# Kernel tuning notes

Hardware: AMD Instinct MI355X
Metric: run time of the kernel (lower is better)

The kernel has to match this reference:

```python
import jax, jax.numpy as jnp
import numpy as np

N_NODES = 100000
N_EDGES = 1600000  # undirected edges (each pair listed once, no self loops)
IN_CH, HID, OUT_CH = 512, 64, 32
MU, P, K = 0.1, 1.5, 2
EPS = 1e-8


def setup_inputs() -> dict:
    key = jax.random.key(0)
    k_x, k_src, k_off, k_w1, k_w2 = jax.random.split(key, 5)
    x = jax.random.normal(k_x, (N_NODES, IN_CH), dtype=jnp.float32)
    # undirected edge list with no self loops: dst = (src + offset) % N, offset in [1, N)
    src = jax.random.randint(k_src, (N_EDGES,), 0, N_NODES)
    off = jax.random.randint(k_off, (N_EDGES,), 1, N_NODES)
    dst = (src + off) % N_NODES
    edge_index = jnp.stack([src, dst], axis=0)
    # parameters (lin1 of pGNNNet, lin1 of pGNNConv)
    W1 = jax.random.normal(k_w1, (IN_CH, HID), dtype=jnp.float32) / np.sqrt(IN_CH)
    b1 = jnp.zeros((HID,), dtype=jnp.float32)
    W2 = jax.random.normal(k_w2, (HID, OUT_CH), dtype=jnp.float32) / np.sqrt(HID)
    b2 = jnp.zeros((OUT_CH,), dtype=jnp.float32)
    return {"x": x, "edge_index": edge_index, "W1": W1, "b1": b1, "W2": W2, "b2": b2}


def reference(x, edge_index, W1, b1, W2, b2):
    src, dst = edge_index[0], edge_index[1]
    n = x.shape[0]
    # pGNNNet.lin1 + ReLU (dropout is identity in eval mode)
    h = jax.nn.relu(x @ W1 + b1)                   # [N, HID]
    # pGNNConv.lin1 applied before propagation
    f = h @ W2 + b2                                # [N, OUT]
    # degrees of the symmetric adjacency (no self loops)
    ones = jnp.ones(src.shape, dtype=f.dtype)
    deg = jax.ops.segment_sum(ones, src, num_segments=n) + \
          jax.ops.segment_sum(ones, dst, num_segments=n)
    dinv = jnp.where(deg > 0, 1.0 / deg, 0.0)      # [N]
    dis = jnp.sqrt(dinv)                           # D^{-1/2}
    out = f
    for _ in range(K):
        gs = out * dis[:, None]                    # D^{-1/2} f
        g = gs[src] - gs[dst]                      # graph gradient per edge [E, OUT]
        # edge reweighting: ||grad||^{p-2}
        w = jnp.power(jnp.sum(g * g, axis=1) + EPS, (P - 2.0) * 0.5)   # [E]
        # row sums of M (symmetric, M_ij = w_e)
        s = jax.ops.segment_sum(w, src, num_segments=n) + \
            jax.ops.segment_sum(w, dst, num_segments=n)
        alpha = 1.0 / (s * dinv + MU)              # [N]
        beta = MU * alpha
        # (D^{-1/2} M D^{-1/2} out): scatter-add messages both directions
        m = w[:, None]
        agg = jax.ops.segment_sum(m * gs[dst], src, num_segments=n) + \
              jax.ops.segment_sum(m * gs[src], dst, num_segments=n)
        out = alpha[:, None] * (dis[:, None] * agg) + beta[:, None] * f
    return jax.nn.log_softmax(out, axis=1)
```

## Files before the change

kernel.cpp:

```cpp
#include <hip/hip_runtime.h>
#include <hip/hip_bf16.h>
#include <math.h>

#define N_NODES 100000
#define N_EDGES 1600000
#define IN_CH 512
#define HID 64
#define OUT_CH 32
#define MU 0.1f
#define EPS 1e-8f

#define HE (2 * N_EDGES)
#define ABLK 625
#define EPT 20
#define NBUCK 391

typedef short bf16x8 __attribute__((ext_vector_type(8)));
typedef unsigned short us8 __attribute__((ext_vector_type(8)));
typedef float f32x4 __attribute__((ext_vector_type(4)));

__device__ __forceinline__ short f2bf(float f) {
  __hip_bfloat16 h = __float2bfloat16(f);
  return *reinterpret_cast<short*>(&h);
}
__device__ __forceinline__ float bf2f(unsigned short u) {
  unsigned int b = ((unsigned int)u) << 16;
  return __uint_as_float(b);
}

__global__ void k_prep(const float* __restrict__ W1, const float* __restrict__ W2,
                       short* __restrict__ w1t, short* __restrict__ w2t) {
  int i = blockIdx.x * 256 + threadIdx.x;
  if (i < IN_CH * HID) {
    int k = i / HID, c = i % HID;
    w1t[c * IN_CH + k] = f2bf(W1[i]);
  } else if (i < IN_CH * HID + HID * OUT_CH) {
    int j = i - IN_CH * HID;
    int k = j / OUT_CH, c = j % OUT_CH;
    w2t[c * HID + k] = f2bf(W2[j]);
  }
}

__global__ __launch_bounds__(256) void k_mlp(
    const float* __restrict__ x, const short* __restrict__ w1t,
    const float* __restrict__ b1, const short* __restrict__ w2t,
    const float* __restrict__ b2, const int* __restrict__ deg,
    float* __restrict__ f, unsigned short* __restrict__ gs) {
  __shared__ short ht[4][16][72];

  const int t = threadIdx.x;
  const int w = t >> 6;
  const int l = t & 63;
  const int lr = l & 15;
  const int kq = l >> 4;

  const int band = blockIdx.x * 64 + w * 16;
  const int gr = band + lr;
  const int grl = gr < N_NODES ? gr : N_NODES - 1;

  f32x4 acc1[4] = {};
  const float* xrow = x + (size_t)grl * IN_CH + kq * 8;
  #pragma unroll 4
  for (int ksub = 0; ksub < 16; ++ksub) {
    float4 alo = *(const float4*)(xrow + ksub * 32);
    float4 ahi = *(const float4*)(xrow + ksub * 32 + 4);
    bf16x8 a;
    a[0] = f2bf(alo.x); a[1] = f2bf(alo.y); a[2] = f2bf(alo.z); a[3] = f2bf(alo.w);
    a[4] = f2bf(ahi.x); a[5] = f2bf(ahi.y); a[6] = f2bf(ahi.z); a[7] = f2bf(ahi.w);
    #pragma unroll
    for (int ct = 0; ct < 4; ++ct) {
      const int c = ct * 16 + lr;
      bf16x8 b = *(const bf16x8*)&w1t[c * IN_CH + ksub * 32 + kq * 8];
      acc1[ct] = __builtin_amdgcn_mfma_f32_16x16x32_bf16(a, b, acc1[ct], 0, 0, 0);
    }
  }

  #pragma unroll
  for (int ct = 0; ct < 4; ++ct) {
    const int c = ct * 16 + lr;
    const float bb = b1[c];
    #pragma unroll
    for (int r = 0; r < 4; ++r) {
      float h = acc1[ct][r] + bb;
      ht[w][kq * 4 + r][c] = f2bf(h > 0.f ? h : 0.f);
    }
  }
  __syncthreads();

  f32x4 acc2[2] = {};
  #pragma unroll
  for (int ks = 0; ks < 2; ++ks) {
    bf16x8 a2 = *(const bf16x8*)&ht[w][lr][ks * 32 + kq * 8];
    #pragma unroll
    for (int ct = 0; ct < 2; ++ct) {
      const int c = ct * 16 + lr;
      bf16x8 b = *(const bf16x8*)&w2t[c * HID + ks * 32 + kq * 8];
      acc2[ct] = __builtin_amdgcn_mfma_f32_16x16x32_bf16(a2, b, acc2[ct], 0, 0, 0);
    }
  }

  #pragma unroll
  for (int r = 0; r < 4; ++r) {
    const int gr2 = band + kq * 4 + r;
    if (gr2 < N_NODES) {
      const int d = deg[gr2];
      const float di = d > 0 ? 1.0f / (float)d : 0.0f;
      const float disv = sqrtf(di);
      #pragma unroll
      for (int ct = 0; ct < 2; ++ct) {
        const int c = ct * 16 + lr;
        const float fv = acc2[ct][r] + b2[c];
        f[(size_t)gr2 * OUT_CH + c] = fv;
        gs[(size_t)gr2 * OUT_CH + c] = (unsigned short)f2bf(fv * disv);
      }
    }
  }
}

__global__ __launch_bounds__(256) void k_bcount(const int* __restrict__ ends,
                                                int* __restrict__ bcnt) {
  __shared__ int cnt[NBUCK];
  for (int i = threadIdx.x; i < NBUCK; i += 256) cnt[i] = 0;
  __syncthreads();
  const int base = blockIdx.x * (256 * EPT);
  #pragma unroll
  for (int j = 0; j < EPT; ++j) {
    int u = ends[base + j * 256 + threadIdx.x];
    atomicAdd(&cnt[u >> 8], 1);
  }
  __syncthreads();
  for (int i = threadIdx.x; i < NBUCK; i += 256) bcnt[i * ABLK + blockIdx.x] = cnt[i];
}

__global__ __launch_bounds__(256) void k_rowsum(const int* __restrict__ bcnt,
                                                int* __restrict__ btotal) {
  const int b = blockIdx.x;
  int s = 0;
  for (int i = threadIdx.x; i < ABLK; i += 256) s += bcnt[b * ABLK + i];
  #pragma unroll
  for (int k = 1; k < 64; k <<= 1) s += __shfl_xor(s, k);
  __shared__ int ws[4];
  if ((threadIdx.x & 63) == 0) ws[threadIdx.x >> 6] = s;
  __syncthreads();
  if (threadIdx.x == 0) btotal[b] = ws[0] + ws[1] + ws[2] + ws[3];
}

__global__ __launch_bounds__(512) void k_bscan(const int* __restrict__ btotal,
                                               int* __restrict__ bucketbase) {
  __shared__ int sh[512];
  const int t = threadIdx.x;
  int v = t < NBUCK ? btotal[t] : 0;
  sh[t] = v;
  __syncthreads();
  for (int s = 1; s < 512; s <<= 1) {
    int a = t >= s ? sh[t - s] : 0;
    __syncthreads();
    sh[t] += a;
    __syncthreads();
  }
  if (t < NBUCK) bucketbase[t] = sh[t] - v;
}

__global__ __launch_bounds__(256) void k_colscan(const int* __restrict__ bcnt,
                                                 const int* __restrict__ bucketbase,
                                                 int* __restrict__ sbase) {
  __shared__ int sh[256];
  const int b = blockIdx.x;
  const int t = threadIdx.x;
  int carry = bucketbase[b];
  for (int c = 0; c < ABLK; c += 256) {
    const int idx = c + t;
    int v = idx < ABLK ? bcnt[b * ABLK + idx] : 0;
    sh[t] = v;
    __syncthreads();
    for (int s = 1; s < 256; s <<= 1) {
      int a = t >= s ? sh[t - s] : 0;
      __syncthreads();
      sh[t] += a;
      __syncthreads();
    }
    if (idx < ABLK) sbase[idx * NBUCK + b] = carry + sh[t] - v;
    carry += sh[255];
    __syncthreads();
  }
}

__global__ __launch_bounds__(256) void k_bscatter(const int* __restrict__ ends,
                                                  const int* __restrict__ sbase,
                                                  int* __restrict__ pairs) {
  __shared__ int cur[NBUCK];
  for (int i = threadIdx.x; i < NBUCK; i += 256)
    cur[i] = sbase[blockIdx.x * NBUCK + i];
  __syncthreads();
  const int base = blockIdx.x * (256 * EPT);
  #pragma unroll
  for (int j = 0; j < EPT; ++j) {
    const int i = base + j * 256 + threadIdx.x;
    const int u = ends[i];
    const int nb = ends[i < N_EDGES ? i + N_EDGES : i - N_EDGES];
    const int slot = atomicAdd(&cur[u >> 8], 1);
    pairs[slot] = ((u & 255) << 24) | nb;
  }
}

__global__ __launch_bounds__(256) void k_csr(const int* __restrict__ pairs,
                                             const int* __restrict__ bucketbase,
                                             const int* __restrict__ btotal,
                                             int* __restrict__ deg,
                                             int* __restrict__ rowstart,
                                             int* __restrict__ adj) {
  __shared__ int cnt[256];
  __shared__ int sh[256];
  const int b = blockIdx.x, t = threadIdx.x;
  const int pbase = bucketbase[b];
  const int psz = btotal[b];
  cnt[t] = 0;
  __syncthreads();
  for (int i = t; i < psz; i += 256)
    atomicAdd(&cnt[((unsigned)pairs[pbase + i]) >> 24], 1);
  __syncthreads();
  const int d = cnt[t];
  sh[t] = d;
  __syncthreads();
  for (int s = 1; s < 256; s <<= 1) {
    int a = t >= s ? sh[t - s] : 0;
    __syncthreads();
    sh[t] += a;
    __syncthreads();
  }
  const int rs = pbase + sh[t] - d;
  const int v = (b << 8) + t;
  if (v < N_NODES) {
    deg[v] = d;
    rowstart[v] = rs;
  }
  __syncthreads();
  cnt[t] = rs;
  __syncthreads();
  for (int i = t; i < psz; i += 256) {
    const int p = pairs[pbase + i];
    adj[atomicAdd(&cnt[((unsigned)p) >> 24], 1)] = p & 0xFFFFFF;
  }
}

template <bool FINAL>
__global__ __launch_bounds__(256) void k_prop(
    const unsigned short* __restrict__ gs_in, const float* __restrict__ f,
    const int* __restrict__ deg, const int* __restrict__ rowstart,
    const int* __restrict__ adj, float* __restrict__ outf,
    unsigned short* __restrict__ outg) {
  const int v = blockIdx.x * 4 + (threadIdx.x >> 6);
  const int lane = threadIdx.x & 63;
  const int slot = lane >> 2;
  const int cg = (lane & 3) << 3;

  const us8 gvu = *(const us8*)&gs_in[v * OUT_CH + cg];
  float gv[8];
  #pragma unroll
  for (int j = 0; j < 8; ++j) gv[j] = bf2f(gvu[j]);

  const int dg = deg[v];
  const float dinvv = dg > 0 ? 1.0f / (float)dg : 0.0f;
  const float disv = sqrtf(dinvv);
  const int i0 = rowstart[v];

  float accs = 0.f;
  float acca[8] = {0.f, 0.f, 0.f, 0.f, 0.f, 0.f, 0.f, 0.f};

  for (int base = 0; base < dg; base += 16) {
    const int idx = base + slot;
    const bool valid = idx < dg;
    const int u = valid ? adj[i0 + idx] : v;
    const us8 guu = *(const us8*)&gs_in[u * OUT_CH + cg];
    float gu[8];
    #pragma unroll
    for (int j = 0; j < 8; ++j) gu[j] = bf2f(guu[j]);
    float d, sq;
    d = gv[0] - gu[0]; sq = d * d;
    #pragma unroll
    for (int j = 1; j < 8; ++j) { d = gv[j] - gu[j]; sq = fmaf(d, d, sq); }
    sq += __shfl_xor(sq, 1);
    sq += __shfl_xor(sq, 2);
    const float w = valid ? __frsqrt_rn(sqrtf(sq + EPS)) : 0.f;
    accs += w;
    #pragma unroll
    for (int j = 0; j < 8; ++j) acca[j] = fmaf(w, gu[j], acca[j]);
  }

  #pragma unroll
  for (int s = 4; s <= 32; s <<= 1) {
    accs += __shfl_xor(accs, s);
    #pragma unroll
    for (int j = 0; j < 8; ++j) acca[j] += __shfl_xor(acca[j], s);
  }

  const float alpha = 1.0f / (accs * dinvv + MU);
  const float ad = alpha * disv;
  const float ba = MU * alpha;
  const float4 fv0 = *(const float4*)&f[v * OUT_CH + cg];
  const float4 fv1 = *(const float4*)&f[v * OUT_CH + cg + 4];
  float r[8];
  r[0] = fmaf(ad, acca[0], ba * fv0.x);
  r[1] = fmaf(ad, acca[1], ba * fv0.y);
  r[2] = fmaf(ad, acca[2], ba * fv0.z);
  r[3] = fmaf(ad, acca[3], ba * fv0.w);
  r[4] = fmaf(ad, acca[4], ba * fv1.x);
  r[5] = fmaf(ad, acca[5], ba * fv1.y);
  r[6] = fmaf(ad, acca[6], ba * fv1.z);
  r[7] = fmaf(ad, acca[7], ba * fv1.w);

  if (FINAL) {
    float m = r[0];
    #pragma unroll
    for (int j = 1; j < 8; ++j) m = fmaxf(m, r[j]);
    m = fmaxf(m, __shfl_xor(m, 1));
    m = fmaxf(m, __shfl_xor(m, 2));
    float se = 0.f;
    #pragma unroll
    for (int j = 0; j < 8; ++j) se += __expf(r[j] - m);
    se += __shfl_xor(se, 1);
    se += __shfl_xor(se, 2);
    const float lse = m + __logf(se);
    if (slot == 0) {
      float4 o0 = make_float4(r[0] - lse, r[1] - lse, r[2] - lse, r[3] - lse);
      float4 o1 = make_float4(r[4] - lse, r[5] - lse, r[6] - lse, r[7] - lse);
      *(float4*)&outf[v * OUT_CH + cg] = o0;
      *(float4*)&outf[v * OUT_CH + cg + 4] = o1;
    }
  } else {
    if (slot == 0) {
      us8 o;
      #pragma unroll
      for (int j = 0; j < 8; ++j) o[j] = (unsigned short)f2bf(r[j] * disv);
      *(us8*)&outg[v * OUT_CH + cg] = o;
    }
  }
}

extern "C" void kernel_launch(void* const* d_in, const int* in_sizes, int n_in,
                              void* d_out, int out_size, void* d_ws, size_t ws_size,
                              hipStream_t stream) {
  const float* x = (const float*)d_in[0];
  const int* ei = (const int*)d_in[1];
  const float* W1 = (const float*)d_in[2];
  const float* b1 = (const float*)d_in[3];
  const float* W2 = (const float*)d_in[4];
  const float* b2 = (const float*)d_in[5];
  float* out = (float*)d_out;

  float* f = (float*)d_ws;
  unsigned short* gsa = (unsigned short*)(f + (size_t)N_NODES * 32);
  unsigned short* gsb = gsa + (size_t)N_NODES * 32;
  int* deg = (int*)(gsb + (size_t)N_NODES * 32);
  int* rowstart = deg + N_NODES;
  int* adj = rowstart + N_NODES;
  short* w1t = (short*)(adj + 2 * N_EDGES);
  short* w2t = w1t + IN_CH * HID;
  int* bcnt = (int*)(w2t + HID * OUT_CH);
  int* sbase = bcnt + NBUCK * ABLK;
  int* btotal = sbase + NBUCK * ABLK;
  int* bucketbase = btotal + NBUCK + 1;
  int* pairs = (int*)f;

  k_prep<<<(IN_CH * HID + HID * OUT_CH + 255) / 256, 256, 0, stream>>>(W1, W2, w1t, w2t);
  k_bcount<<<ABLK, 256, 0, stream>>>(ei, bcnt);
  k_rowsum<<<NBUCK, 256, 0, stream>>>(bcnt, btotal);
  k_bscan<<<1, 512, 0, stream>>>(btotal, bucketbase);
  k_colscan<<<NBUCK, 256, 0, stream>>>(bcnt, bucketbase, sbase);
  k_bscatter<<<ABLK, 256, 0, stream>>>(ei, sbase, pairs);
  k_csr<<<NBUCK, 256, 0, stream>>>(pairs, bucketbase, btotal, deg, rowstart, adj);
  k_mlp<<<(N_NODES + 63) / 64, 256, 0, stream>>>(x, w1t, b1, w2t, b2, deg, f, gsa);
  k_prop<false><<<N_NODES / 4, 256, 0, stream>>>(gsa, f, deg, rowstart, adj, nullptr, gsb);
  k_prop<true><<<N_NODES / 4, 256, 0, stream>>>(gsb, f, deg, rowstart, adj, out, nullptr);
}
```

Baseline: 291.4 us.

## Fuse CSR build stages into one cooperative kernel with grid syncs

Replaces seven small kernels (weight prep, bucket count, row sum, bucket scan, column scan, scatter, CSR fill) with a single cooperative kernel of 625 blocks that uses grid.sync between phases. The aim is to remove per-kernel launch gaps and tail drain between the small stages. The cost is grid-wide barrier overhead and the requirement that all 625 blocks be co-resident. The bucket scan now runs in a 256-wide block with a carry loop instead of a 512-wide block.

```diff
diff --git a/kernel.cpp b/kernel.cpp
--- a/kernel.cpp
+++ b/kernel.cpp
@@ -1,6 +1,9 @@
 #include <hip/hip_runtime.h>
 #include <hip/hip_bf16.h>
+#include <hip/hip_cooperative_groups.h>
 #include <math.h>
+
+namespace cg = cooperative_groups;
 
 #define N_NODES 100000
 #define N_EDGES 1600000
@@ -28,16 +31,146 @@
   return __uint_as_float(b);
 }
 
-__global__ void k_prep(const float* __restrict__ W1, const float* __restrict__ W2,
-                       short* __restrict__ w1t, short* __restrict__ w2t) {
-  int i = blockIdx.x * 256 + threadIdx.x;
-  if (i < IN_CH * HID) {
-    int k = i / HID, c = i % HID;
-    w1t[c * IN_CH + k] = f2bf(W1[i]);
-  } else if (i < IN_CH * HID + HID * OUT_CH) {
-    int j = i - IN_CH * HID;
-    int k = j / OUT_CH, c = j % OUT_CH;
-    w2t[c * HID + k] = f2bf(W2[j]);
+__global__ __launch_bounds__(256) void k_build(
+    const int* __restrict__ ends, const float* __restrict__ W1,
+    const float* __restrict__ W2, short* __restrict__ w1t,
+    short* __restrict__ w2t, int* __restrict__ bcnt, int* __restrict__ btotal,
+    int* __restrict__ bucketbase, int* __restrict__ sbase,
+    int* __restrict__ pairs, int* __restrict__ deg, int* __restrict__ rowstart,
+    int* __restrict__ adj) {
+  cg::grid_group grid = cg::this_grid();
+  __shared__ int cnt[NBUCK];
+  __shared__ int sh[256];
+  __shared__ int ws[4];
+  const int t = threadIdx.x;
+  const int b = blockIdx.x;
+
+  {
+    const int i = b * 256 + t;
+    if (i < IN_CH * HID) {
+      int k = i / HID, c = i % HID;
+      w1t[c * IN_CH + k] = f2bf(W1[i]);
+    } else if (i < IN_CH * HID + HID * OUT_CH) {
+      int j = i - IN_CH * HID;
+      w2t[(j % OUT_CH) * HID + (j / OUT_CH)] = f2bf(W2[j]);
+    }
+  }
+
+  for (int i = t; i < NBUCK; i += 256) cnt[i] = 0;
+  __syncthreads();
+  {
+    const int base = b * (256 * EPT);
+    #pragma unroll
+    for (int j = 0; j < EPT; ++j) {
+      int u = ends[base + j * 256 + t];
+      atomicAdd(&cnt[u >> 8], 1);
+    }
+  }
+  __syncthreads();
+  for (int i = t; i < NBUCK; i += 256) bcnt[i * ABLK + b] = cnt[i];
+
+  grid.sync();
+
+  if (b < NBUCK) {
+    int s = 0;
+    for (int i = t; i < ABLK; i += 256) s += bcnt[b * ABLK + i];
+    #pragma unroll
+    for (int k = 1; k < 64; k <<= 1) s += __shfl_xor(s, k);
+    if ((t & 63) == 0) ws[t >> 6] = s;
+    __syncthreads();
+    if (t == 0) btotal[b] = ws[0] + ws[1] + ws[2] + ws[3];
+  }
+
+  grid.sync();
+
+  if (b == 0) {
+    int carry = 0;
+    for (int c0 = 0; c0 < NBUCK; c0 += 256) {
+      const int idx = c0 + t;
+      int v = idx < NBUCK ? btotal[idx] : 0;
+      sh[t] = v;
+      __syncthreads();
+      for (int s = 1; s < 256; s <<= 1) {
+        int a = t >= s ? sh[t - s] : 0;
+        __syncthreads();
+        sh[t] += a;
+        __syncthreads();
+      }
+      if (idx < NBUCK) bucketbase[idx] = carry + sh[t] - v;
+      carry += sh[255];
+      __syncthreads();
+    }
+  }
+
+  grid.sync();
+
+  if (b < NBUCK) {
+    int carry = bucketbase[b];
+    for (int c0 = 0; c0 < ABLK; c0 += 256) {
+      const int idx = c0 + t;
+      int v = idx < ABLK ? bcnt[b * ABLK + idx] : 0;
+      sh[t] = v;
+      __syncthreads();
+      for (int s = 1; s < 256; s <<= 1) {
+        int a = t >= s ? sh[t - s] : 0;
+        __syncthreads();
+        sh[t] += a;
+        __syncthreads();
+      }
+      if (idx < ABLK) sbase[idx * NBUCK + b] = carry + sh[t] - v;
+      carry += sh[255];
+      __syncthreads();
+    }
+  }
+
+  grid.sync();
+
+  for (int i = t; i < NBUCK; i += 256) cnt[i] = sbase[b * NBUCK + i];
+  __syncthreads();
+  {
+    const int base = b * (256 * EPT);
+    #pragma unroll
+    for (int j = 0; j < EPT; ++j) {
+      const int i = base + j * 256 + t;
+      const int u = ends[i];
+      const int nb2 = ends[i < N_EDGES ? i + N_EDGES : i - N_EDGES];
+      const int slot = atomicAdd(&cnt[u >> 8], 1);
+      pairs[slot] = ((u & 255) << 24) | nb2;
+    }
+  }
+
+  grid.sync();
+
+  if (b < NBUCK) {
+    const int pbase = bucketbase[b];
+    const int psz = btotal[b];
+    cnt[t] = 0;
+    __syncthreads();
+    for (int i = t; i < psz; i += 256)
+      atomicAdd(&cnt[((unsigned)pairs[pbase + i]) >> 24], 1);
+    __syncthreads();
+    const int d = cnt[t];
+    sh[t] = d;
+    __syncthreads();
+    for (int s = 1; s < 256; s <<= 1) {
+      int a = t >= s ? sh[t - s] : 0;
+      __syncthreads();
+      sh[t] += a;
+      __syncthreads();
+    }
+    const int rs = pbase + sh[t] - d;
+    const int v = (b << 8) + t;
+    if (v < N_NODES) {
+      deg[v] = d;
+      rowstart[v] = rs;
+    }
+    __syncthreads();
+    cnt[t] = rs;
+    __syncthreads();
+    for (int i = t; i < psz; i += 256) {
+      const int p = pairs[pbase + i];
+      adj[atomicAdd(&cnt[((unsigned)p) >> 24], 1)] = p & 0xFFFFFF;
+    }
   }
 }
 
@@ -70,8 +203,8 @@
     #pragma unroll
     for (int ct = 0; ct < 4; ++ct) {
       const int c = ct * 16 + lr;
-      bf16x8 b = *(const bf16x8*)&w1t[c * IN_CH + ksub * 32 + kq * 8];
-      acc1[ct] = __builtin_amdgcn_mfma_f32_16x16x32_bf16(a, b, acc1[ct], 0, 0, 0);
+      bf16x8 bfrag = *(const bf16x8*)&w1t[c * IN_CH + ksub * 32 + kq * 8];
+      acc1[ct] = __builtin_amdgcn_mfma_f32_16x16x32_bf16(a, bfrag, acc1[ct], 0, 0, 0);
     }
   }
 
@@ -94,8 +227,8 @@
     #pragma unroll
     for (int ct = 0; ct < 2; ++ct) {
       const int c = ct * 16 + lr;
-      bf16x8 b = *(const bf16x8*)&w2t[c * HID + ks * 32 + kq * 8];
-      acc2[ct] = __builtin_amdgcn_mfma_f32_16x16x32_bf16(a2, b, acc2[ct], 0, 0, 0);
+      bf16x8 bfrag = *(const bf16x8*)&w2t[c * HID + ks * 32 + kq * 8];
+      acc2[ct] = __builtin_amdgcn_mfma_f32_16x16x32_bf16(a2, bfrag, acc2[ct], 0, 0, 0);
     }
   }
 
@@ -117,132 +250,6 @@
   }
 }
 
-__global__ __launch_bounds__(256) void k_bcount(const int* __restrict__ ends,
-                                                int* __restrict__ bcnt) {
-  __shared__ int cnt[NBUCK];
-  for (int i = threadIdx.x; i < NBUCK; i += 256) cnt[i] = 0;
-  __syncthreads();
-  const int base = blockIdx.x * (256 * EPT);
-  #pragma unroll
-  for (int j = 0; j < EPT; ++j) {
-    int u = ends[base + j * 256 + threadIdx.x];
-    atomicAdd(&cnt[u >> 8], 1);
-  }
-  __syncthreads();
-  for (int i = threadIdx.x; i < NBUCK; i += 256) bcnt[i * ABLK + blockIdx.x] = cnt[i];
-}
-
-__global__ __launch_bounds__(256) void k_rowsum(const int* __restrict__ bcnt,
-                                                int* __restrict__ btotal) {
-  const int b = blockIdx.x;
-  int s = 0;
-  for (int i = threadIdx.x; i < ABLK; i += 256) s += bcnt[b * ABLK + i];
-  #pragma unroll
-  for (int k = 1; k < 64; k <<= 1) s += __shfl_xor(s, k);
-  __shared__ int ws[4];
-  if ((threadIdx.x & 63) == 0) ws[threadIdx.x >> 6] = s;
-  __syncthreads();
-  if (threadIdx.x == 0) btotal[b] = ws[0] + ws[1] + ws[2] + ws[3];
-}
-
-__global__ __launch_bounds__(512) void k_bscan(const int* __restrict__ btotal,
-                                               int* __restrict__ bucketbase) {
-  __shared__ int sh[512];
-  const int t = threadIdx.x;
-  int v = t < NBUCK ? btotal[t] : 0;
-  sh[t] = v;
-  __syncthreads();
-  for (int s = 1; s < 512; s <<= 1) {
-    int a = t >= s ? sh[t - s] : 0;
-    __syncthreads();
-    sh[t] += a;
-    __syncthreads();
-  }
-  if (t < NBUCK) bucketbase[t] = sh[t] - v;
-}
-
-__global__ __launch_bounds__(256) void k_colscan(const int* __restrict__ bcnt,
-                                                 const int* __restrict__ bucketbase,
-                                                 int* __restrict__ sbase) {
-  __shared__ int sh[256];
-  const int b = blockIdx.x;
-  const int t = threadIdx.x;
-  int carry = bucketbase[b];
-  for (int c = 0; c < ABLK; c += 256) {
-    const int idx = c + t;
-    int v = idx < ABLK ? bcnt[b * ABLK + idx] : 0;
-    sh[t] = v;
-    __syncthreads();
-    for (int s = 1; s < 256; s <<= 1) {
-      int a = t >= s ? sh[t - s] : 0;
-      __syncthreads();
-      sh[t] += a;
-      __syncthreads();
-    }
-    if (idx < ABLK) sbase[idx * NBUCK + b] = carry + sh[t] - v;
-    carry += sh[255];
-    __syncthreads();
-  }
-}
-
-__global__ __launch_bounds__(256) void k_bscatter(const int* __restrict__ ends,
-                                                  const int* __restrict__ sbase,
-                                                  int* __restrict__ pairs) {
-  __shared__ int cur[NBUCK];
-  for (int i = threadIdx.x; i < NBUCK; i += 256)
-    cur[i] = sbase[blockIdx.x * NBUCK + i];
-  __syncthreads();
-  const int base = blockIdx.x * (256 * EPT);
-  #pragma unroll
-  for (int j = 0; j < EPT; ++j) {
-    const int i = base + j * 256 + threadIdx.x;
-    const int u = ends[i];
-    const int nb = ends[i < N_EDGES ? i + N_EDGES : i - N_EDGES];
-    const int slot = atomicAdd(&cur[u >> 8], 1);
-    pairs[slot] = ((u & 255) << 24) | nb;
-  }
-}
-
-__global__ __launch_bounds__(256) void k_csr(const int* __restrict__ pairs,
-                                             const int* __restrict__ bucketbase,
-                                             const int* __restrict__ btotal,
-                                             int* __restrict__ deg,
-                                             int* __restrict__ rowstart,
-                                             int* __restrict__ adj) {
-  __shared__ int cnt[256];
-  __shared__ int sh[256];
-  const int b = blockIdx.x, t = threadIdx.x;
-  const int pbase = bucketbase[b];
-  const int psz = btotal[b];
-  cnt[t] = 0;
-  __syncthreads();
-  for (int i = t; i < psz; i += 256)
-    atomicAdd(&cnt[((unsigned)pairs[pbase + i]) >> 24], 1);
-  __syncthreads();
-  const int d = cnt[t];
-  sh[t] = d;
-  __syncthreads();
-  for (int s = 1; s < 256; s <<= 1) {
-    int a = t >= s ? sh[t - s] : 0;
-    __syncthreads();
-    sh[t] += a;
-    __syncthreads();
-  }
-  const int rs = pbase + sh[t] - d;
-  const int v = (b << 8) + t;
-  if (v < N_NODES) {
-    deg[v] = d;
-    rowstart[v] = rs;
-  }
-  __syncthreads();
-  cnt[t] = rs;
-  __syncthreads();
-  for (int i = t; i < psz; i += 256) {
-    const int p = pairs[pbase + i];
-    adj[atomicAdd(&cnt[((unsigned)p) >> 24], 1)] = p & 0xFFFFFF;
-  }
-}
-
 template <bool FINAL>
 __global__ __launch_bounds__(256) void k_prop(
     const unsigned short* __restrict__ gs_in, const float* __restrict__ f,
@@ -252,9 +259,9 @@
   const int v = blockIdx.x * 4 + (threadIdx.x >> 6);
   const int lane = threadIdx.x & 63;
   const int slot = lane >> 2;
-  const int cg = (lane & 3) << 3;
-
-  const us8 gvu = *(const us8*)&gs_in[v * OUT_CH + cg];
+  const int cg2 = (lane & 3) << 3;
+
+  const us8 gvu = *(const us8*)&gs_in[v * OUT_CH + cg2];
   float gv[8];
   #pragma unroll
   for (int j = 0; j < 8; ++j) gv[j] = bf2f(gvu[j]);
@@ -271,7 +278,7 @@
     const int idx = base + slot;
     const bool valid = idx < dg;
     const int u = valid ? adj[i0 + idx] : v;
-    const us8 guu = *(const us8*)&gs_in[u * OUT_CH + cg];
+    const us8 guu = *(const us8*)&gs_in[u * OUT_CH + cg2];
     float gu[8];
     #pragma unroll
     for (int j = 0; j < 8; ++j) gu[j] = bf2f(guu[j]);
@@ -297,8 +304,8 @@
   const float alpha = 1.0f / (accs * dinvv + MU);
   const float ad = alpha * disv;
   const float ba = MU * alpha;
-  const float4 fv0 = *(const float4*)&f[v * OUT_CH + cg];
-  const float4 fv1 = *(const float4*)&f[v * OUT_CH + cg + 4];
+  const float4 fv0 = *(const float4*)&f[v * OUT_CH + cg2];
+  const float4 fv1 = *(const float4*)&f[v * OUT_CH + cg2 + 4];
   float r[8];
   r[0] = fmaf(ad, acca[0], ba * fv0.x);
   r[1] = fmaf(ad, acca[1], ba * fv0.y);
@@ -324,15 +331,15 @@
     if (slot == 0) {
       float4 o0 = make_float4(r[0] - lse, r[1] - lse, r[2] - lse, r[3] - lse);
       float4 o1 = make_float4(r[4] - lse, r[5] - lse, r[6] - lse, r[7] - lse);
-      *(float4*)&outf[v * OUT_CH + cg] = o0;
-      *(float4*)&outf[v * OUT_CH + cg + 4] = o1;
+      *(float4*)&outf[v * OUT_CH + cg2] = o0;
+      *(float4*)&outf[v * OUT_CH + cg2 + 4] = o1;
     }
   } else {
     if (slot == 0) {
       us8 o;
       #pragma unroll
       for (int j = 0; j < 8; ++j) o[j] = (unsigned short)f2bf(r[j] * disv);
-      *(us8*)&outg[v * OUT_CH + cg] = o;
+      *(us8*)&outg[v * OUT_CH + cg2] = o;
     }
   }
 }
@@ -362,13 +369,11 @@
   int* bucketbase = btotal + NBUCK + 1;
   int* pairs = (int*)f;
 
-  k_prep<<<(IN_CH * HID + HID * OUT_CH + 255) / 256, 256, 0, stream>>>(W1, W2, w1t, w2t);
-  k_bcount<<<ABLK, 256, 0, stream>>>(ei, bcnt);
-  k_rowsum<<<NBUCK, 256, 0, stream>>>(bcnt, btotal);
-  k_bscan<<<1, 512, 0, stream>>>(btotal, bucketbase);
-  k_colscan<<<NBUCK, 256, 0, stream>>>(bcnt, bucketbase, sbase);
-  k_bscatter<<<ABLK, 256, 0, stream>>>(ei, sbase, pairs);
-  k_csr<<<NBUCK, 256, 0, stream>>>(pairs, bucketbase, btotal, deg, rowstart, adj);
+  void* args[] = {(void*)&ei, (void*)&W1, (void*)&W2, (void*)&w1t, (void*)&w2t,
+                  (void*)&bcnt, (void*)&btotal, (void*)&bucketbase, (void*)&sbase,
+                  (void*)&pairs, (void*)&deg, (void*)&rowstart, (void*)&adj};
+  hipLaunchCooperativeKernel(reinterpret_cast<void*>(k_build), dim3(ABLK),
+                             dim3(256), args, 0, stream);
   k_mlp<<<(N_NODES + 63) / 64, 256, 0, stream>>>(x, w1t, b1, w2t, b2, deg, f, gsa);
   k_prop<false><<<N_NODES / 4, 256, 0, stream>>>(gsa, f, deg, rowstart, adj, nullptr, gsb);
   k_prop<true><<<N_NODES / 4, 256, 0, stream>>>(gsb, f, deg, rowstart, adj, out, nullptr);
```

After: 661.1 us. +126.9%, slower.
